# Performance work log

Hardware: AMD Instinct MI355X
Metric: run time of the kernel (lower is better)

## Reference

```python
import jax, jax.numpy as jnp
import numpy as np

B, T, F_IN = 64, 512, 264        # batch, time, total features
NONLSTM = 8                      # trailing non-LSTM feature channels
F_LSTM = F_IN - NONLSTM          # 256 features fed to the LSTM stack
HIDDEN = [512, 512]              # stacked OptimizedLSTMCell dims
DENSE = [512, 256]
PRED, FPP = 16, 4                # predictions, features_per_prediction


def _glorot(key, shape):
    fan_in, fan_out = shape[0], shape[1]
    lim = jnp.sqrt(6.0 / (fan_in + fan_out))
    return jax.random.uniform(key, shape, jnp.float32, -lim, lim)


def setup_inputs() -> dict:
    key = jax.random.key(0)
    ks = jax.random.split(key, 16)
    inp = {"x": jax.random.normal(ks[0], (B, T, F_IN), jnp.float32)}
    # LSTM layer params: Wi [in,4H] (no bias on input proj), Wh [H,4H], b [4H]
    in_dim = F_LSTM
    for j, h in enumerate(HIDDEN):
        inp[f"Wi{j}"] = _glorot(ks[1 + 3 * j], (in_dim, 4 * h))
        inp[f"Wh{j}"] = _glorot(ks[2 + 3 * j], (h, 4 * h))
        inp[f"b{j}"] = jnp.zeros((4 * h,), jnp.float32)
        in_dim = h
    # Dense head
    d_in = HIDDEN[-1] + NONLSTM
    for i, d in enumerate(DENSE):
        inp[f"Wd{i}"] = _glorot(ks[8 + 2 * i], (d_in, d))
        inp[f"bd{i}"] = jnp.zeros((d,), jnp.float32)
        d_in = d
    inp["Wf"] = _glorot(ks[14], (d_in, PRED * FPP))
    inp["bf"] = jnp.zeros((PRED * FPP,), jnp.float32)
    return inp


def lstm_layer(x, Wi, Wh, b):
    """flax OptimizedLSTMCell scanned over time. x: [B, T, F] -> [B, T, H]."""
    Bq = x.shape[0]
    H = Wh.shape[0]
    xw = jnp.einsum('btf,fg->btg', x, Wi)  # precompute input projections

    def step(carry, z_in):
        c, h = carry
        z = z_in + h @ Wh + b
        i, f, g, o = jnp.split(z, 4, axis=-1)
        c = jax.nn.sigmoid(f) * c + jax.nn.sigmoid(i) * jnp.tanh(g)
        h = jax.nn.sigmoid(o) * jnp.tanh(c)
        return (c, h), h

    c0 = jnp.zeros((Bq, H), x.dtype)
    h0 = jnp.zeros((Bq, H), x.dtype)
    _, hs = jax.lax.scan(step, (c0, h0), jnp.swapaxes(xw, 0, 1))
    return jnp.swapaxes(hs, 0, 1)


def reference(x, Wi0, Wh0, b0, Wi1, Wh1, b1, Wd0, bd0, Wd1, bd1, Wf, bf):
    last_features = x[:, -1, -NONLSTM:]          # [B, 8]
    h = x[:, :, :-NONLSTM]                       # [B, T, 256]
    # single LSTM branch: history == T, downsample == 1
    h = lstm_layer(h, Wi0, Wh0, b0)
    h = lstm_layer(h, Wi1, Wh1, b1)
    out = h[:, -1, :]                            # [B, H]
    out = jnp.concatenate([out, last_features], axis=1)
    out = jax.nn.relu(out @ Wd0 + bd0)
    out = jax.nn.relu(out @ Wd1 + bd1)
    out = out @ Wf + bf
    out = out.reshape((-1, PRED, FPP))
    return jax.nn.sigmoid(out)
```

## Files before the change

### kernel.cpp

```cpp
#include <hip/hip_runtime.h>
#include <hip/hip_bf16.h>

typedef __hip_bfloat16 bf16;
typedef short bf16x8 __attribute__((ext_vector_type(8)));
typedef float f32x4 __attribute__((ext_vector_type(4)));
typedef unsigned long long u64;
typedef unsigned int u32;

#define MFMA16(A, B, C) __builtin_amdgcn_mfma_f32_16x16x32_bf16(A, B, C, 0, 0, 0)

__device__ __forceinline__ float sigf(float x) { return 1.f / (1.f + __expf(-x)); }
__device__ __forceinline__ float tanh_fast(float x) { return 2.f / (1.f + __expf(-2.f * x)) - 1.f; }

__device__ __forceinline__ bf16x8 ld16(const u64* p) {
  u64 lo = __hip_atomic_load(p, __ATOMIC_RELAXED, __HIP_MEMORY_SCOPE_SYSTEM);
  u64 hi = __hip_atomic_load(p + 1, __ATOMIC_RELAXED, __HIP_MEMORY_SCOPE_SYSTEM);
  union { u64 q[2]; bf16x8 v; } u;
  u.q[0] = lo; u.q[1] = hi;
  return u.v;
}

__global__ __launch_bounds__(256) void transpose_k(const float* __restrict__ W,
                                                   bf16* __restrict__ WT,
                                                   int K, int N) {
  __shared__ bf16 tile[32][33];
  const int n0 = blockIdx.x * 32, k0 = blockIdx.y * 32;
  const int c = threadIdx.x & 31, r0 = threadIdx.x >> 5;
  for (int i = 0; i < 4; ++i) {
    int r = r0 + 8 * i;
    tile[r][c] = __float2bfloat16(W[(long)(k0 + r) * N + (n0 + c)]);
  }
  __syncthreads();
  for (int i = 0; i < 4; ++i) {
    int r = r0 + 8 * i;
    WT[(long)(n0 + r) * K + (k0 + c)] = tile[c][r];
  }
}

__device__ __forceinline__ void gather16(const u64* __restrict__ mat, int m, int q,
                                         bf16x8* out) {
#pragma unroll
  for (int i = 0; i < 16; ++i) {
    const int s = i * 4 + q;
    out[i] = *(const bf16x8*)(mat + ((long)(s << 6) + m) * 2);
  }
}

__global__ __launch_bounds__(256, 1) void lstm2_fused_k(
    const float* __restrict__ x,
    const bf16* __restrict__ WiT0, const bf16* __restrict__ WhT0,
    const float* __restrict__ bias0,
    const bf16* __restrict__ WiT1, const bf16* __restrict__ WhT1,
    const float* __restrict__ bias1,
    u64* __restrict__ h1D, u64* __restrict__ h2D,
    u32* __restrict__ sent)
{
  __shared__ short Wis[32 * 520];
  __shared__ short Whs[32 * 520];
  __shared__ float zs[32 * 66];
  __shared__ __align__(16) bf16 hstage[64 * 8];

  const int layer = blockIdx.x >> 6;
  const int w = blockIdx.x & 63;
  const int tid = threadIdx.x;
  const int lane = tid & 63;
  const int wv = tid >> 6;
  const int q = lane >> 4;
  const int r = lane & 15;

  if (tid == 0) asm volatile("buffer_inv sc0 sc1" ::: "memory");

  const int K_in = layer ? 512 : 256;
  const bf16* WiT = layer ? WiT1 : WiT0;
  const bf16* WhT = layer ? WhT1 : WhT0;
  const float* bias = layer ? bias1 : bias0;
  u32* s0 = sent;
  u32* s1 = sent + 512 * 64;
  u64* houtD = layer ? h2D : h1D;
  u32* smy = (layer ? s1 : s0);

  for (int idx = tid; idx < 32 * 64; idx += 256) {
    const int j = idx >> 6, kc = idx & 63;
    const int zc = (j >> 3) * 512 + w * 8 + (j & 7);
    *(bf16x8*)(Whs + j * 520 + kc * 8) = *(const bf16x8*)(WhT + (long)zc * 512 + kc * 8);
  }
  const int csh = layer ? 6 : 5;
  const int cmask = (1 << csh) - 1;
  for (int idx = tid; idx < (32 << csh); idx += 256) {
    const int j = idx >> csh, kc = idx & cmask;
    const int zc = (j >> 3) * 512 + w * 8 + (j & 7);
    *(bf16x8*)(Wis + j * 520 + kc * 8) = *(const bf16x8*)(WiT + (long)zc * K_in + kc * 8);
  }

  const int m = wv * 16 + r;
  const short* wi0p = Wis + r * 520;
  const short* wi1p = Wis + (16 + r) * 520;
  const short* wh0p = Whs + r * 520;
  const short* wh1p = Whs + (16 + r) * 520;

  const int gb = tid & 63;
  const int gc0 = tid >> 6;
  float bias_r[2][4];
  for (int s = 0; s < 2; ++s)
    for (int g = 0; g < 4; ++g)
      bias_r[s][g] = bias[g * 512 + w * 8 + gc0 + 4 * s];
  float creg[2] = {0.f, 0.f};

  __syncthreads();

  for (int t = 0; t < 512; ++t) {
    f32x4 acc0 = {0.f, 0.f, 0.f, 0.f};
    f32x4 acc1 = {0.f, 0.f, 0.f, 0.f};

    if (layer == 0) {
      bf16x8 ax[8];
      const float* row = x + ((long)m * 512 + t) * 264;
#pragma unroll
      for (int i = 0; i < 8; ++i) {
        const float4 f0 = *(const float4*)(row + i * 32 + q * 8);
        const float4 f1 = *(const float4*)(row + i * 32 + q * 8 + 4);
        union { short s[8]; bf16x8 v8; } o;
        o.s[0] = __builtin_bit_cast(short, __float2bfloat16(f0.x));
        o.s[1] = __builtin_bit_cast(short, __float2bfloat16(f0.y));
        o.s[2] = __builtin_bit_cast(short, __float2bfloat16(f0.z));
        o.s[3] = __builtin_bit_cast(short, __float2bfloat16(f0.w));
        o.s[4] = __builtin_bit_cast(short, __float2bfloat16(f1.x));
        o.s[5] = __builtin_bit_cast(short, __float2bfloat16(f1.y));
        o.s[6] = __builtin_bit_cast(short, __float2bfloat16(f1.z));
        o.s[7] = __builtin_bit_cast(short, __float2bfloat16(f1.w));
        ax[i] = o.v8;
      }
#pragma unroll
      for (int i = 0; i < 8; ++i) {
        const int kk = i * 32;
        acc0 = MFMA16(ax[i], *(const bf16x8*)(wi0p + kk + q * 8), acc0);
        acc1 = MFMA16(ax[i], *(const bf16x8*)(wi1p + kk + q * 8), acc1);
      }
      if (t > 0) {
        if (tid < 64) {
          const u32* sp = s0 + (t - 1) * 64 + tid;
          while (__ballot(__hip_atomic_load(sp, __ATOMIC_RELAXED,
                                            __HIP_MEMORY_SCOPE_SYSTEM) != 0) != ~0ull)
            __builtin_amdgcn_s_sleep(2);
        }
        __syncthreads();
        bf16x8 ah[16];
        gather16(h1D + (long)(t - 1) * 8192, m, q, ah);
#pragma unroll
        for (int i = 0; i < 16; ++i) {
          const int kk = i * 32;
          acc0 = MFMA16(ah[i], *(const bf16x8*)(wh0p + kk + q * 8), acc0);
          acc1 = MFMA16(ah[i], *(const bf16x8*)(wh1p + kk + q * 8), acc1);
        }
      }
    } else {
      if (tid < 64) {
        const u32* sp = s0 + t * 64 + tid;
        while (__ballot(__hip_atomic_load(sp, __ATOMIC_RELAXED,
                                          __HIP_MEMORY_SCOPE_SYSTEM) != 0) != ~0ull)
          __builtin_amdgcn_s_sleep(2);
      }
      __syncthreads();
      bf16x8 ax[16];
      gather16(h1D + (long)t * 8192, m, q, ax);
#pragma unroll
      for (int i = 0; i < 16; ++i) {
        const int kk = i * 32;
        acc0 = MFMA16(ax[i], *(const bf16x8*)(wi0p + kk + q * 8), acc0);
        acc1 = MFMA16(ax[i], *(const bf16x8*)(wi1p + kk + q * 8), acc1);
      }
      if (t > 0) {
        if (tid < 64) {
          const u32* sp = s1 + (t - 1) * 64 + tid;
          while (__ballot(__hip_atomic_load(sp, __ATOMIC_RELAXED,
                                            __HIP_MEMORY_SCOPE_SYSTEM) != 0) != ~0ull)
            __builtin_amdgcn_s_sleep(2);
        }
        __syncthreads();
        bf16x8 ah[16];
        gather16(h2D + (long)(t - 1) * 8192, m, q, ah);
#pragma unroll
        for (int i = 0; i < 16; ++i) {
          const int kk = i * 32;
          acc0 = MFMA16(ah[i], *(const bf16x8*)(wh0p + kk + q * 8), acc0);
          acc1 = MFMA16(ah[i], *(const bf16x8*)(wh1p + kk + q * 8), acc1);
        }
      }
    }

    {
      const int brow = wv * 16 + q * 4;
      for (int i = 0; i < 4; ++i) zs[r * 66 + brow + i] = acc0[i];
      for (int i = 0; i < 4; ++i) zs[(16 + r) * 66 + brow + i] = acc1[i];
    }
    __syncthreads();

    for (int s = 0; s < 2; ++s) {
      const int c = gc0 + 4 * s;
      const float zi = zs[(c)*66 + gb] + bias_r[s][0];
      const float zf = zs[(8 + c) * 66 + gb] + bias_r[s][1];
      const float zg = zs[(16 + c) * 66 + gb] + bias_r[s][2];
      const float zo = zs[(24 + c) * 66 + gb] + bias_r[s][3];
      const float cnew = sigf(zf) * creg[s] + sigf(zi) * tanh_fast(zg);
      const float hnew = sigf(zo) * tanh_fast(cnew);
      creg[s] = cnew;
      hstage[gb * 8 + c] = __float2bfloat16(hnew);
    }
    __syncthreads();

    if (tid < 64) {
      const u64* src = (const u64*)(hstage + tid * 8);
      u64* dst = houtD + (((long)t * 64 + w) * 64 + tid) * 2;
      __hip_atomic_store(dst, src[0], __ATOMIC_RELAXED, __HIP_MEMORY_SCOPE_SYSTEM);
      __hip_atomic_store(dst + 1, src[1], __ATOMIC_RELAXED, __HIP_MEMORY_SCOPE_SYSTEM);
    }
    if (tid == 0)
      __hip_atomic_store(smy + t * 64 + w, 1u, __ATOMIC_RELEASE, __HIP_MEMORY_SCOPE_AGENT);
  }
}

__global__ __launch_bounds__(256) void head_k(
    const u64* __restrict__ h2D,
    const float* __restrict__ x,
    const float* __restrict__ Wd0, const float* __restrict__ bd0,
    const float* __restrict__ Wd1, const float* __restrict__ bd1,
    const float* __restrict__ Wf, const float* __restrict__ bfv,
    float* __restrict__ out) {
  const int b = blockIdx.x, tid = threadIdx.x;
  __shared__ float in0[520];
  __shared__ float d0s[512];
  __shared__ float d1s[256];
  if (tid < 64) {
    const int s = tid;
    bf16x8 v = ld16(h2D + (((long)511 * 64 + s) * 64 + b) * 2);
    union { bf16x8 v8; short sh[8]; } u;
    u.v8 = v;
    for (int j = 0; j < 8; ++j)
      in0[s * 8 + j] = __bfloat162float(__builtin_bit_cast(bf16, u.sh[j]));
  }
  if (tid < 8) in0[512 + tid] = x[((long)(b * 512 + 511)) * 264 + 256 + tid];
  __syncthreads();
  for (int j = tid; j < 512; j += 256) {
    float a = bd0[j];
    for (int k = 0; k < 520; ++k) a += in0[k] * Wd0[(long)k * 512 + j];
    d0s[j] = fmaxf(a, 0.f);
  }
  __syncthreads();
  if (tid < 256) {
    const int j = tid;
    float a = bd1[j];
    for (int k = 0; k < 512; ++k) a += d0s[k] * Wd1[(long)k * 256 + j];
    d1s[j] = fmaxf(a, 0.f);
  }
  __syncthreads();
  if (tid < 64) {
    const int j = tid;
    float a = bfv[j];
    for (int k = 0; k < 256; ++k) a += d1s[k] * Wf[(long)k * 64 + j];
    out[b * 64 + j] = sigf(a);
  }
}

extern "C" void kernel_launch(void* const* d_in, const int* in_sizes, int n_in,
                              void* d_out, int out_size, void* d_ws, size_t ws_size,
                              hipStream_t stream) {
  const float* x   = (const float*)d_in[0];
  const float* Wi0 = (const float*)d_in[1];
  const float* Wh0 = (const float*)d_in[2];
  const float* b0  = (const float*)d_in[3];
  const float* Wi1 = (const float*)d_in[4];
  const float* Wh1 = (const float*)d_in[5];
  const float* b1  = (const float*)d_in[6];
  const float* Wd0 = (const float*)d_in[7];
  const float* bd0 = (const float*)d_in[8];
  const float* Wd1 = (const float*)d_in[9];
  const float* bd1 = (const float*)d_in[10];
  const float* Wf  = (const float*)d_in[11];
  const float* bf_ = (const float*)d_in[12];
  float* out = (float*)d_out;

  char* ws = (char*)d_ws;
  size_t off = 0;
  auto carve = [&](size_t bytes) {
    void* p = ws + off;
    off += (bytes + 255) & ~(size_t)255;
    return p;
  };
  u32* sent = (u32*)carve((size_t)2 * 512 * 64 * 4);
  const size_t zero_bytes = off;
  bf16* WiT0 = (bf16*)carve((size_t)2048 * 256 * 2);
  bf16* WhT0 = (bf16*)carve((size_t)2048 * 512 * 2);
  bf16* WiT1 = (bf16*)carve((size_t)2048 * 512 * 2);
  bf16* WhT1 = (bf16*)carve((size_t)2048 * 512 * 2);
  u64*  h1D  = (u64*)carve((size_t)512 * 64 * 64 * 16);
  u64*  h2D  = (u64*)carve((size_t)512 * 64 * 64 * 16);

  (void)hipMemsetAsync(sent, 0, zero_bytes, stream);

  transpose_k<<<dim3(2048 / 32, 256 / 32), 256, 0, stream>>>(Wi0, WiT0, 256, 2048);
  transpose_k<<<dim3(2048 / 32, 512 / 32), 256, 0, stream>>>(Wh0, WhT0, 512, 2048);
  transpose_k<<<dim3(2048 / 32, 512 / 32), 256, 0, stream>>>(Wi1, WiT1, 512, 2048);
  transpose_k<<<dim3(2048 / 32, 512 / 32), 256, 0, stream>>>(Wh1, WhT1, 512, 2048);

  lstm2_fused_k<<<128, 256, 0, stream>>>(x, WiT0, WhT0, b0, WiT1, WhT1, b1,
                                         h1D, h2D, sent);

  head_k<<<64, 256, 0, stream>>>(h2D, x, Wd0, bd0, Wd1, bd1, Wf, bf_, out);
}
```

Measured before the change: 2.735 ms.

## Use per-wave flags and in-register gate math to remove block barriers

Each wave now polls its own per-wave readiness flags and publishes its 16 batch rows with its own flag, so sentinels become per (timestep, wave, block) and the workspace grows fourfold. Gate pre-activations are paired with an xor-8 lane shuffle instead of going through a shared-memory z buffer, so the LSTM cell update is done directly in registers. Together these remove all __syncthreads from the per-timestep loop and shorten the serial critical path of the recurrence. The cost is four times more flag polling and stores, and half the lanes sit idle during the cell math. The hstage write and read within a wave rely on wave-level ordering rather than an explicit barrier.

```diff
diff --git a/kernel.cpp b/kernel.cpp
--- a/kernel.cpp
+++ b/kernel.cpp
@@ -44,6 +44,12 @@
     const int s = i * 4 + q;
     out[i] = *(const bf16x8*)(mat + ((long)(s << 6) + m) * 2);
   }
+}
+
+__device__ __forceinline__ void pollplane(const u32* sp) {
+  while (__ballot(__hip_atomic_load(sp, __ATOMIC_RELAXED,
+                                    __HIP_MEMORY_SCOPE_SYSTEM) != 0) != ~0ull)
+    __builtin_amdgcn_s_sleep(1);
 }
 
 __global__ __launch_bounds__(256, 1) void lstm2_fused_k(
@@ -57,7 +63,6 @@
 {
   __shared__ short Wis[32 * 520];
   __shared__ short Whs[32 * 520];
-  __shared__ float zs[32 * 66];
   __shared__ __align__(16) bf16 hstage[64 * 8];
 
   const int layer = blockIdx.x >> 6;
@@ -75,7 +80,7 @@
   const bf16* WhT = layer ? WhT1 : WhT0;
   const float* bias = layer ? bias1 : bias0;
   u32* s0 = sent;
-  u32* s1 = sent + 512 * 64;
+  u32* s1 = sent + 512 * 4 * 64;
   u64* houtD = layer ? h2D : h1D;
   u32* smy = (layer ? s1 : s0);
 
@@ -98,13 +103,10 @@
   const short* wh0p = Whs + r * 520;
   const short* wh1p = Whs + (16 + r) * 520;
 
-  const int gb = tid & 63;
-  const int gc0 = tid >> 6;
-  float bias_r[2][4];
-  for (int s = 0; s < 2; ++s)
-    for (int g = 0; g < 4; ++g)
-      bias_r[s][g] = bias[g * 512 + w * 8 + gc0 + 4 * s];
-  float creg[2] = {0.f, 0.f};
+  float br4[4];
+#pragma unroll
+  for (int g = 0; g < 4; ++g) br4[g] = bias[g * 512 + w * 8 + (r & 7)];
+  float creg[4] = {0.f, 0.f, 0.f, 0.f};
 
   __syncthreads();
 
@@ -137,13 +139,7 @@
         acc1 = MFMA16(ax[i], *(const bf16x8*)(wi1p + kk + q * 8), acc1);
       }
       if (t > 0) {
-        if (tid < 64) {
-          const u32* sp = s0 + (t - 1) * 64 + tid;
-          while (__ballot(__hip_atomic_load(sp, __ATOMIC_RELAXED,
-                                            __HIP_MEMORY_SCOPE_SYSTEM) != 0) != ~0ull)
-            __builtin_amdgcn_s_sleep(2);
-        }
-        __syncthreads();
+        pollplane(s0 + ((long)(t - 1) * 4 + wv) * 64 + lane);
         bf16x8 ah[16];
         gather16(h1D + (long)(t - 1) * 8192, m, q, ah);
 #pragma unroll
@@ -154,13 +150,7 @@
         }
       }
     } else {
-      if (tid < 64) {
-        const u32* sp = s0 + t * 64 + tid;
-        while (__ballot(__hip_atomic_load(sp, __ATOMIC_RELAXED,
-                                          __HIP_MEMORY_SCOPE_SYSTEM) != 0) != ~0ull)
-          __builtin_amdgcn_s_sleep(2);
-      }
-      __syncthreads();
+      pollplane(s0 + ((long)t * 4 + wv) * 64 + lane);
       bf16x8 ax[16];
       gather16(h1D + (long)t * 8192, m, q, ax);
 #pragma unroll
@@ -170,13 +160,7 @@
         acc1 = MFMA16(ax[i], *(const bf16x8*)(wi1p + kk + q * 8), acc1);
       }
       if (t > 0) {
-        if (tid < 64) {
-          const u32* sp = s1 + (t - 1) * 64 + tid;
-          while (__ballot(__hip_atomic_load(sp, __ATOMIC_RELAXED,
-                                            __HIP_MEMORY_SCOPE_SYSTEM) != 0) != ~0ull)
-            __builtin_amdgcn_s_sleep(2);
-        }
-        __syncthreads();
+        pollplane(s1 + ((long)(t - 1) * 4 + wv) * 64 + lane);
         bf16x8 ah[16];
         gather16(h2D + (long)(t - 1) * 8192, m, q, ah);
 #pragma unroll
@@ -188,34 +172,35 @@
       }
     }
 
-    {
-      const int brow = wv * 16 + q * 4;
-      for (int i = 0; i < 4; ++i) zs[r * 66 + brow + i] = acc0[i];
-      for (int i = 0; i < 4; ++i) zs[(16 + r) * 66 + brow + i] = acc1[i];
-    }
-    __syncthreads();
-
-    for (int s = 0; s < 2; ++s) {
-      const int c = gc0 + 4 * s;
-      const float zi = zs[(c)*66 + gb] + bias_r[s][0];
-      const float zf = zs[(8 + c) * 66 + gb] + bias_r[s][1];
-      const float zg = zs[(16 + c) * 66 + gb] + bias_r[s][2];
-      const float zo = zs[(24 + c) * 66 + gb] + bias_r[s][3];
-      const float cnew = sigf(zf) * creg[s] + sigf(zi) * tanh_fast(zg);
-      const float hnew = sigf(zo) * tanh_fast(cnew);
-      creg[s] = cnew;
-      hstage[gb * 8 + c] = __float2bfloat16(hnew);
-    }
-    __syncthreads();
-
-    if (tid < 64) {
-      const u64* src = (const u64*)(hstage + tid * 8);
-      u64* dst = houtD + (((long)t * 64 + w) * 64 + tid) * 2;
-      __hip_atomic_store(dst, src[0], __ATOMIC_RELAXED, __HIP_MEMORY_SCOPE_SYSTEM);
-      __hip_atomic_store(dst + 1, src[1], __ATOMIC_RELAXED, __HIP_MEMORY_SCOPE_SYSTEM);
-    }
-    if (tid == 0)
-      __hip_atomic_store(smy + t * 64 + w, 1u, __ATOMIC_RELEASE, __HIP_MEMORY_SCOPE_AGENT);
+    f32x4 accf, acco;
+#pragma unroll
+    for (int i = 0; i < 4; ++i) {
+      accf[i] = __shfl_xor(acc0[i], 8, 64);
+      acco[i] = __shfl_xor(acc1[i], 8, 64);
+    }
+    if (r < 8) {
+#pragma unroll
+      for (int i = 0; i < 4; ++i) {
+        const float zi = acc0[i] + br4[0];
+        const float zf = accf[i] + br4[1];
+        const float zg = acc1[i] + br4[2];
+        const float zo = acco[i] + br4[3];
+        const float cnew = sigf(zf) * creg[i] + sigf(zi) * tanh_fast(zg);
+        const float hnew = sigf(zo) * tanh_fast(cnew);
+        creg[i] = cnew;
+        hstage[(wv * 16 + q * 4 + i) * 8 + r] = __float2bfloat16(hnew);
+      }
+    }
+    if (lane < 16) {
+      const u64* src = (const u64*)(hstage + (wv * 16 + lane) * 8);
+      const u64 d0 = src[0], d1 = src[1];
+      u64* dst = houtD + (((long)t * 64 + w) * 64 + (wv * 16 + lane)) * 2;
+      __hip_atomic_store(dst, d0, __ATOMIC_RELAXED, __HIP_MEMORY_SCOPE_SYSTEM);
+      __hip_atomic_store(dst + 1, d1, __ATOMIC_RELAXED, __HIP_MEMORY_SCOPE_SYSTEM);
+      if (lane == 0)
+        __hip_atomic_store(smy + ((long)t * 4 + wv) * 64 + w, 1u,
+                           __ATOMIC_RELEASE, __HIP_MEMORY_SCOPE_AGENT);
+    }
   }
 }
 
@@ -286,7 +271,7 @@
     off += (bytes + 255) & ~(size_t)255;
     return p;
   };
-  u32* sent = (u32*)carve((size_t)2 * 512 * 64 * 4);
+  u32* sent = (u32*)carve((size_t)2 * 512 * 4 * 64 * 4);
   const size_t zero_bytes = off;
   bf16* WiT0 = (bf16*)carve((size_t)2048 * 256 * 2);
   bf16* WhT0 = (bf16*)carve((size_t)2048 * 512 * 2);
```

Result: slower. 5.426 ms (+98.4%).
